# Kernel optimization log

Hardware: AMD Instinct MI355X
Metric: run time of the kernel (lower is better)

The kernel has to match this reference:

```python
import jax, jax.numpy as jnp
import numpy as np

B, D = 8, 36          # batch, spatial extent of each of the 4 dims
KOUT = D - 2          # VALID conv with kernel 3 -> 34

_DN = jax.lax.ConvDimensionNumbers(lhs_spec=(0, 1, 2, 3, 4, 5),
                                   rhs_spec=(0, 1, 2, 3, 4, 5),
                                   out_spec=(0, 1, 2, 3, 4, 5))

def _conv4d(x, w):
    # x: [B, Cin, D,D,D,D], w: [Cout, Cin, 3,3,3,3] -> [B, Cout, D-2,...]
    return jax.lax.conv_general_dilated(x, w, window_strides=(1, 1, 1, 1),
                                        padding='VALID', dimension_numbers=_DN)

def setup_inputs() -> dict:
    key = jax.random.key(0)
    ks = jax.random.split(key, 8)
    fan_in = 1 * 3 ** 4  # 81 taps
    return {
        'x_real': jax.random.normal(ks[0], (B, 1, D, D, D, D), jnp.float32),
        'x_imag': jax.random.normal(ks[1], (B, 1, D, D, D, D), jnp.float32),
        'w_real': jax.random.normal(ks[2], (2, 1, 3, 3, 3, 3), jnp.float32) / np.sqrt(fan_in),
        'w_imag': jax.random.normal(ks[3], (2, 1, 3, 3, 3, 3), jnp.float32) / np.sqrt(fan_in),
        'b_real': jax.random.normal(ks[4], (2,), jnp.float32) * 0.1,
        'b_imag': jax.random.normal(ks[5], (2,), jnp.float32) * 0.1,
        'head_w': jax.random.normal(ks[6], (1, KOUT), jnp.float32) / np.sqrt(KOUT),
        'head_b': jax.random.normal(ks[7], (1,), jnp.float32) * 0.1,
    }

def reference(x_real, x_imag, w_real, w_imag, b_real, b_imag, head_w, head_b):
    bshape = (1, -1, 1, 1, 1, 1)
    # complex 4D conv: (Wr + iWi) * (xr + ixi)
    yr = _conv4d(x_real, w_real) - _conv4d(x_imag, w_imag) + b_real.reshape(bshape)
    yi = _conv4d(x_real, w_imag) + _conv4d(x_imag, w_real) + b_imag.reshape(bshape)
    # CReLU: ReLU on real and imaginary parts independently
    yr = jax.nn.relu(yr)
    yi = jax.nn.relu(yi)
    # Modulus (tiny eps keeps grad finite at 0, matching practical impls)
    m = jnp.sqrt(yr * yr + yi * yi + 1e-12)  # [B, 2, 34,34,34,34]
    # Linear(out=1) over the last spatial dim, then sigmoid
    h = jnp.einsum('bcdefw,ow->bcdefo', m, head_w) + head_b
    out = jax.nn.sigmoid(h)[:, 0]  # drop channel dim -> [B, 34, 34, 34, 1]
    return out
```

## Files before the change

kernel.cpp:

```cpp
#include <hip/hip_runtime.h>
#include <hip/hip_fp16.h>
#include <math.h>

namespace {
constexpr int DIN = 36, DOUT = 34;
constexpr int RT = 6;
constexpr int NROWS = RT*RT*RT;
constexpr int ROWW  = 38;
constexpr int NCHUNK = NROWS*9;
constexpr int NTILE = 9;
constexpr int BLOCKS_PER_B = NTILE*NTILE*NTILE;
constexpr int NBLOCKS = 8*BLOCKS_PER_B;
constexpr int NT = 512;
constexpr int SITER = (NCHUNK + NT - 1)/NT;
constexpr int D3 = DIN*DIN*DIN, D2 = DIN*DIN;
constexpr int WS_WPK  = 0;
constexpr int WS_SCAL = 216;
constexpr int WS_HW   = 220;
}

__device__ __forceinline__ unsigned div9u(unsigned n) { return __umulhi(n, 0x38E38E39u) >> 1; }
__device__ __forceinline__ unsigned div6u(unsigned n) { return __umulhi(n, 0xAAAAAAABu) >> 2; }

__device__ __forceinline__ unsigned pack2h(float a, float b) {
    union { __half2 h; unsigned u; } x; x.h = __floats2half2_rn(a, b); return x.u;
}
__device__ __forceinline__ __half2 bch(unsigned u) {
    union { unsigned u; __half2 h; } x; x.u = u; return x.h;
}

__global__ void prep_kernel(const float* __restrict__ wr, const float* __restrict__ wi,
                            const float* __restrict__ br, const float* __restrict__ bi,
                            const float* __restrict__ hw, const float* __restrict__ hb,
                            unsigned* __restrict__ ws)
{
    const int t = threadIdx.x;
    if (t < 27) {
        uint4* p = reinterpret_cast<uint4*>(ws + WS_WPK);
        p[2*t]   = make_uint4(pack2h(wr[3*t],   -wi[3*t]),
                              pack2h(wr[3*t+1], -wi[3*t+1]),
                              pack2h(wr[3*t+2], -wi[3*t+2]), 0u);
        p[2*t+1] = make_uint4(pack2h(wi[3*t],    wr[3*t]),
                              pack2h(wi[3*t+1],  wr[3*t+1]),
                              pack2h(wi[3*t+2],  wr[3*t+2]), 0u);
    }
    if (t < DOUT) reinterpret_cast<float*>(ws)[WS_HW + t] = hw[t];
    if (t == 63) {
        float* s = reinterpret_cast<float*>(ws);
        s[WS_SCAL] = br[0]; s[WS_SCAL+1] = bi[0]; s[WS_SCAL+2] = hb[0];
    }
}

__device__ __forceinline__ void stage(const float* __restrict__ xr, const float* __restrict__ xi,
                                      unsigned* __restrict__ s_xu, int t, unsigned g0off)
{
    #pragma unroll
    for (int it = 0; it < SITER; ++it) {
        const int C = it*NT + t;
        if (C < NCHUNK) {
            const unsigned row = div9u((unsigned)C);
            const unsigned c   = (unsigned)C - row*9u;
            const unsigned rd  = div9u(row) >> 2;
            const unsigned rem = row - rd*36u;
            const unsigned re  = div6u(rem);
            const unsigned rf  = rem - re*6u;
            const unsigned goff = g0off + rd*D3 + re*D2 + rf*DIN + c*4u;
            const float4 vr = *reinterpret_cast<const float4*>(xr + goff);
            const float4 vi = *reinterpret_cast<const float4*>(xi + goff);
            unsigned* dst = s_xu + row*ROWW + c*4;
            uint2 lo, hi;
            lo.x = pack2h(vr.x, vi.x); lo.y = pack2h(vr.y, vi.y);
            hi.x = pack2h(vr.z, vi.z); hi.y = pack2h(vr.w, vi.w);
            *reinterpret_cast<uint2*>(dst)     = lo;
            *reinterpret_cast<uint2*>(dst + 2) = hi;
        }
    }
}

template<int NW, int W0>
__device__ __forceinline__ float conv_group(const unsigned* __restrict__ s_xu,
                                            const uint4* __restrict__ wpk,
                                            const float* __restrict__ hws,
                                            int d, int e, int f,
                                            float c_br, float c_bi, float hinit)
{
    constexpr int NL = (NW + 2)/2;
    __half2 accr[NW], acci[NW];
    #pragma unroll
    for (int w = 0; w < NW; ++w) {
        accr[w] = __floats2half2_rn(0.f, 0.f);
        acci[w] = __floats2half2_rn(0.f, 0.f);
    }

    #pragma unroll 1
    for (int i = 0; i < 3; ++i)
    #pragma unroll 1
    for (int j = 0; j < 3; ++j)
    {
        const unsigned* sp = s_xu + (((d+i)*RT + (e+j))*RT + f)*ROWW + W0;
        const int tapb = (i*3 + j)*3;
        #pragma unroll
        for (int k = 0; k < 3; ++k)
        {
            uint2 q[NL];
            #pragma unroll
            for (int m = 0; m < NL; ++m)
                q[m] = *reinterpret_cast<const uint2*>(sp + k*ROWW + 2*m);
            const __half2* win = reinterpret_cast<const __half2*>(q);

            const uint4 wa = wpk[2*(tapb + k)];
            const uint4 wb = wpk[2*(tapb + k) + 1];
            #pragma unroll
            for (int l = 0; l < 3; ++l) {
                const __half2 WA = bch(l==0 ? wa.x : l==1 ? wa.y : wa.z);
                const __half2 WB = bch(l==0 ? wb.x : l==1 ? wb.y : wb.z);
                #pragma unroll
                for (int w = 0; w < NW; ++w) {
                    const __half2 x2 = win[w + l];
                    accr[w] = __hfma2(x2, WA, accr[w]);
                    acci[w] = __hfma2(x2, WB, acci[w]);
                }
            }
        }
    }

    float h = hinit;
    #pragma unroll
    for (int w = 0; w < NW; ++w) {
        const float yr = __low2float(accr[w]) + __high2float(accr[w]) + c_br;
        const float yi = __low2float(acci[w]) + __high2float(acci[w]) + c_bi;
        const float a = fmaxf(yr, 0.f);
        const float c = fmaxf(yi, 0.f);
        const float m = sqrtf(fmaf(a, a, fmaf(c, c, 1e-12f)));
        h = fmaf(m, hws[W0 + w], h);
    }
    return h;
}

__global__ __launch_bounds__(NT)
void lasl_kernel(const float* __restrict__ xr, const float* __restrict__ xi,
                 const unsigned* __restrict__ wsu, float* __restrict__ out)
{
    __shared__ unsigned s_xu[NROWS*ROWW];
    __shared__ float s_red[NT];

    const int t = threadIdx.x;

    const int bid = blockIdx.x;
    const int b   = bid & 7;
    int rem = bid >> 3;
    const int dt = rem / 81;  rem -= dt*81;
    const int et = rem / 9;
    const int ft = rem - (rem/9)*9;
    const int d0 = min(4*dt, 30);
    const int e0 = min(4*et, 30);
    const int f0 = min(4*ft, 30);

    const float* xrb = xr + (size_t)b * (size_t)(DIN*D3);
    const float* xib = xi + (size_t)b * (size_t)(DIN*D3);
    const unsigned g0off = (unsigned)((d0*DIN + e0)*DIN + f0)*DIN;

    stage(xrb, xib, s_xu, t, g0off);
    __syncthreads();

    const int f = t & 3;
    const int e = (t >> 2) & 3;
    const int d = (t >> 4) & 3;
    const int g = t >> 6;

    const uint4* wpk  = reinterpret_cast<const uint4*>(wsu + WS_WPK);
    const float* scal = reinterpret_cast<const float*>(wsu);
    const float* hws  = scal + WS_HW;
    const float c_br = scal[WS_SCAL], c_bi = scal[WS_SCAL+1];
    const float hini = (g == 0) ? scal[WS_SCAL+2] : 0.f;

    float hp;
    if      (g == 0) hp = conv_group<6, 0>(s_xu, wpk, hws, d, e, f, c_br, c_bi, hini);
    else if (g == 1) hp = conv_group<4, 6>(s_xu, wpk, hws, d, e, f, c_br, c_bi, hini);
    else if (g == 2) hp = conv_group<4,10>(s_xu, wpk, hws, d, e, f, c_br, c_bi, hini);
    else if (g == 3) hp = conv_group<4,14>(s_xu, wpk, hws, d, e, f, c_br, c_bi, hini);
    else if (g == 4) hp = conv_group<4,18>(s_xu, wpk, hws, d, e, f, c_br, c_bi, hini);
    else if (g == 5) hp = conv_group<4,22>(s_xu, wpk, hws, d, e, f, c_br, c_bi, hini);
    else if (g == 6) hp = conv_group<4,26>(s_xu, wpk, hws, d, e, f, c_br, c_bi, hini);
    else             hp = conv_group<4,30>(s_xu, wpk, hws, d, e, f, c_br, c_bi, hini);

    __syncthreads();
    s_red[t] = hp;
    __syncthreads();

    if (g == 0) {
        float htot = hp;
        #pragma unroll
        for (int gg = 1; gg < 8; ++gg) htot += s_red[t + 64*gg];
        out[(((size_t)b*DOUT + (d0 + d))*DOUT + (e0 + e))*DOUT + (f0 + f)] =
            1.f / (1.f + __expf(-htot));
    }
}

extern "C" void kernel_launch(void* const* d_in, const int* in_sizes, int n_in,
                              void* d_out, int out_size, void* d_ws, size_t ws_size,
                              hipStream_t stream)
{
    const float* xr = (const float*)d_in[0];
    const float* xi = (const float*)d_in[1];
    const float* wr = (const float*)d_in[2];
    const float* wi = (const float*)d_in[3];
    const float* br = (const float*)d_in[4];
    const float* bi = (const float*)d_in[5];
    const float* hw = (const float*)d_in[6];
    const float* hb = (const float*)d_in[7];
    float* out = (float*)d_out;
    unsigned* ws = (unsigned*)d_ws;

    prep_kernel<<<1, 64, 0, stream>>>(wr, wi, br, bi, hw, hb, ws);
    lasl_kernel<<<NBLOCKS, NT, 0, stream>>>(xr, xi, ws, out);
}
```

Before: 90.74 us.

## Enlarge spatial tiles to 5x5x5 and split width into four thread groups

Switches from 4x4x4 output tiles (6^3 halo rows) to 5x5x5 tiles (7^3 halo rows), which cuts halo overhead and the block count. Each thread now computes 8-9 width outputs across 4 groups instead of 4-6 across 8 groups, so each loaded window is reused for more outputs and the cross-group reduction is shorter. Handling odd width offsets requires base/offset indexing. In exchange, shared memory grows, 3 of every 128 threads are idle, and per-thread register use rises because of the larger accumulator arrays.

Result: slower. 92.94 us (+2.4%).

```diff
diff --git a/kernel.cpp b/kernel.cpp
--- a/kernel.cpp
+++ b/kernel.cpp
@@ -4,11 +4,12 @@
 
 namespace {
 constexpr int DIN = 36, DOUT = 34;
-constexpr int RT = 6;
+constexpr int TS = 5;
+constexpr int RT = 7;
 constexpr int NROWS = RT*RT*RT;
 constexpr int ROWW  = 38;
 constexpr int NCHUNK = NROWS*9;
-constexpr int NTILE = 9;
+constexpr int NTILE = 7;
 constexpr int BLOCKS_PER_B = NTILE*NTILE*NTILE;
 constexpr int NBLOCKS = 8*BLOCKS_PER_B;
 constexpr int NT = 512;
@@ -20,7 +21,6 @@
 }
 
 __device__ __forceinline__ unsigned div9u(unsigned n) { return __umulhi(n, 0x38E38E39u) >> 1; }
-__device__ __forceinline__ unsigned div6u(unsigned n) { return __umulhi(n, 0xAAAAAAABu) >> 2; }
 
 __device__ __forceinline__ unsigned pack2h(float a, float b) {
     union { __half2 h; unsigned u; } x; x.h = __floats2half2_rn(a, b); return x.u;
@@ -60,10 +60,10 @@
         if (C < NCHUNK) {
             const unsigned row = div9u((unsigned)C);
             const unsigned c   = (unsigned)C - row*9u;
-            const unsigned rd  = div9u(row) >> 2;
-            const unsigned rem = row - rd*36u;
-            const unsigned re  = div6u(rem);
-            const unsigned rf  = rem - re*6u;
+            const unsigned rd  = (row*1338u) >> 16;
+            const unsigned rem = row - rd*49u;
+            const unsigned re  = (rem*9363u) >> 16;
+            const unsigned rf  = rem - re*7u;
             const unsigned goff = g0off + rd*D3 + re*D2 + rf*DIN + c*4u;
             const float4 vr = *reinterpret_cast<const float4*>(xr + goff);
             const float4 vi = *reinterpret_cast<const float4*>(xi + goff);
@@ -84,7 +84,9 @@
                                             int d, int e, int f,
                                             float c_br, float c_bi, float hinit)
 {
-    constexpr int NL = (NW + 2)/2;
+    constexpr int BASE   = W0 & ~1;
+    constexpr int IDXOFF = W0 & 1;
+    constexpr int NL = (IDXOFF + NW + 2 + 1)/2;
     __half2 accr[NW], acci[NW];
     #pragma unroll
     for (int w = 0; w < NW; ++w) {
@@ -97,7 +99,7 @@
     #pragma unroll 1
     for (int j = 0; j < 3; ++j)
     {
-        const unsigned* sp = s_xu + (((d+i)*RT + (e+j))*RT + f)*ROWW + W0;
+        const unsigned* sp = s_xu + (((d+i)*RT + (e+j))*RT + f)*ROWW + BASE;
         const int tapb = (i*3 + j)*3;
         #pragma unroll
         for (int k = 0; k < 3; ++k)
@@ -116,7 +118,7 @@
                 const __half2 WB = bch(l==0 ? wb.x : l==1 ? wb.y : wb.z);
                 #pragma unroll
                 for (int w = 0; w < NW; ++w) {
-                    const __half2 x2 = win[w + l];
+                    const __half2 x2 = win[IDXOFF + w + l];
                     accr[w] = __hfma2(x2, WA, accr[w]);
                     acci[w] = __hfma2(x2, WB, acci[w]);
                 }
@@ -149,12 +151,12 @@
     const int bid = blockIdx.x;
     const int b   = bid & 7;
     int rem = bid >> 3;
-    const int dt = rem / 81;  rem -= dt*81;
-    const int et = rem / 9;
-    const int ft = rem - (rem/9)*9;
-    const int d0 = min(4*dt, 30);
-    const int e0 = min(4*et, 30);
-    const int f0 = min(4*ft, 30);
+    const int dt = rem / 49;  rem -= dt*49;
+    const int et = rem / 7;
+    const int ft = rem - et*7;
+    const int d0 = min(5*dt, 29);
+    const int e0 = min(5*et, 29);
+    const int f0 = min(5*ft, 29);
 
     const float* xrb = xr + (size_t)b * (size_t)(DIN*D3);
     const float* xib = xi + (size_t)b * (size_t)(DIN*D3);
@@ -163,10 +165,12 @@
     stage(xrb, xib, s_xu, t, g0off);
     __syncthreads();
 
-    const int f = t & 3;
-    const int e = (t >> 2) & 3;
-    const int d = (t >> 4) & 3;
-    const int g = t >> 6;
+    const int s  = min(t & 127, 124);
+    const int sv = (t & 127) < 125;
+    const int f  = s % 5;
+    const int e  = (s / 5) % 5;
+    const int d  = s / 25;
+    const int g  = t >> 7;
 
     const uint4* wpk  = reinterpret_cast<const uint4*>(wsu + WS_WPK);
     const float* scal = reinterpret_cast<const float*>(wsu);
@@ -175,23 +179,16 @@
     const float hini = (g == 0) ? scal[WS_SCAL+2] : 0.f;
 
     float hp;
-    if      (g == 0) hp = conv_group<6, 0>(s_xu, wpk, hws, d, e, f, c_br, c_bi, hini);
-    else if (g == 1) hp = conv_group<4, 6>(s_xu, wpk, hws, d, e, f, c_br, c_bi, hini);
-    else if (g == 2) hp = conv_group<4,10>(s_xu, wpk, hws, d, e, f, c_br, c_bi, hini);
-    else if (g == 3) hp = conv_group<4,14>(s_xu, wpk, hws, d, e, f, c_br, c_bi, hini);
-    else if (g == 4) hp = conv_group<4,18>(s_xu, wpk, hws, d, e, f, c_br, c_bi, hini);
-    else if (g == 5) hp = conv_group<4,22>(s_xu, wpk, hws, d, e, f, c_br, c_bi, hini);
-    else if (g == 6) hp = conv_group<4,26>(s_xu, wpk, hws, d, e, f, c_br, c_bi, hini);
-    else             hp = conv_group<4,30>(s_xu, wpk, hws, d, e, f, c_br, c_bi, hini);
-
-    __syncthreads();
+    if      (g == 0) hp = conv_group<9, 0>(s_xu, wpk, hws, d, e, f, c_br, c_bi, hini);
+    else if (g == 1) hp = conv_group<8, 9>(s_xu, wpk, hws, d, e, f, c_br, c_bi, hini);
+    else if (g == 2) hp = conv_group<9,17>(s_xu, wpk, hws, d, e, f, c_br, c_bi, hini);
+    else             hp = conv_group<8,26>(s_xu, wpk, hws, d, e, f, c_br, c_bi, hini);
+
     s_red[t] = hp;
     __syncthreads();
 
-    if (g == 0) {
-        float htot = hp;
-        #pragma unroll
-        for (int gg = 1; gg < 8; ++gg) htot += s_red[t + 64*gg];
+    if (g == 0 && sv) {
+        const float htot = hp + s_red[t + 128] + s_red[t + 256] + s_red[t + 384];
         out[(((size_t)b*DOUT + (d0 + d))*DOUT + (e0 + e))*DOUT + (f0 + f)] =
             1.f / (1.f + __expf(-htot));
     }
```
